# Optimization experiments

Hardware: AMD Instinct MI355X
Metric: run time of the kernel (lower is better)

The kernel has to match this reference:

```python
import jax, jax.numpy as jnp
import numpy as np

B, S, D, H, HD, MLP = 2, 4096, 512, 8, 64, 2048
BLK, C = 128, 32  # Fixed1Pattern(block_size=128), Fixed2Pattern(block_size=128, c=32)
EPS = 1e-6


def _xavier(key, shape, fan_in, fan_out):
    lim = np.sqrt(6.0 / (fan_in + fan_out)).astype(np.float32)
    return jax.random.uniform(key, shape, jnp.float32, -lim, lim)


def setup_inputs() -> dict:
    key = jax.random.key(0)
    ks = jax.random.split(key, 9)
    return {
        "inputs": jax.random.normal(ks[0], (B, S, D), jnp.float32),
        "ln1_scale": jnp.ones((D,), jnp.float32),
        "ln1_bias": jnp.zeros((D,), jnp.float32),
        "wq": _xavier(ks[1], (D, H, HD), D, H * HD),
        "wk": _xavier(ks[2], (D, H, HD), D, H * HD),
        "wv": _xavier(ks[3], (D, H, HD), D, H * HD),
        "wo": _xavier(ks[4], (H, HD, D), H * HD, D),
        "ln2_scale": jnp.ones((D,), jnp.float32),
        "ln2_bias": jnp.zeros((D,), jnp.float32),
        "w1": _xavier(ks[5], (D, MLP), D, MLP),
        "b1": jax.random.normal(ks[6], (MLP,), jnp.float32) * 1e-6,
        "w2": _xavier(ks[7], (MLP, D), MLP, D),
        "b2": jax.random.normal(ks[8], (D,), jnp.float32) * 1e-6,
    }


def _layer_norm(x, scale, bias):
    mu = jnp.mean(x, axis=-1, keepdims=True)
    var = jnp.mean(jnp.square(x - mu), axis=-1, keepdims=True)
    return (x - mu) * jax.lax.rsqrt(var + EPS) * scale + bias


def _sparse_mask():
    # Union of causal Fixed1 (same block) and Fixed2 (last C columns of each block) patterns.
    i = jnp.arange(S)[:, None]
    j = jnp.arange(S)[None, :]
    causal = j <= i
    local = (i // BLK) == (j // BLK)            # Fixed1: within-block
    strided = (j % BLK) >= (BLK - C)            # Fixed2: block-summary columns
    return causal & (local | strided)           # [S, S] bool


def reference(inputs, ln1_scale, ln1_bias, wq, wk, wv, wo,
              ln2_scale, ln2_bias, w1, b1, w2, b2):
    x = _layer_norm(inputs, ln1_scale, ln1_bias)
    q = jnp.einsum("bsd,dhk->bshk", x, wq)
    k = jnp.einsum("bsd,dhk->bshk", x, wk)
    v = jnp.einsum("bsd,dhk->bshk", x, wv)
    scale = 1.0 / np.sqrt(HD).astype(np.float32)
    scores = jnp.einsum("bqhk,bshk->bhqs", q * scale, k)  # [B,H,S,S]
    mask = _sparse_mask()[None, None]
    scores = jnp.where(mask, scores, jnp.float32(-1e9))
    attn = jax.nn.softmax(scores, axis=-1)
    ctx = jnp.einsum("bhqs,bshk->bqhk", attn, v)
    attn_out = jnp.einsum("bqhk,hkd->bqd", ctx, wo)
    x = attn_out + inputs  # residual 1 (dropout deterministic)
    y = _layer_norm(x, ln2_scale, ln2_bias)
    y = jax.nn.gelu(y @ w1 + b1) @ w2 + b2  # MlpBlock
    return x + y
```

## Files before the change

kernel.cpp:

```cpp
#include <hip/hip_runtime.h>
#include <hip/hip_bf16.h>

typedef __attribute__((ext_vector_type(8))) __bf16 bf16x8;
typedef __attribute__((ext_vector_type(8))) short s16x8;
typedef __attribute__((ext_vector_type(4))) float f32x4;

#define NB 2
#define NS 4096
#define ND 512
#define NH 8
#define NHD 64
#define NMLP 2048

__device__ __forceinline__ unsigned short f2b(float f) {
  __hip_bfloat16 h = __float2bfloat16(f);
  return __builtin_bit_cast(unsigned short, h);
}

__device__ __forceinline__ float geluf(float x) {
  float u = 0.7978845608028654f * (x + 0.044715f * x * x * x);
  return x / (1.0f + __expf(-2.0f * u));
}

__device__ __forceinline__ void gload16(const void* g, void* l) {
  __builtin_amdgcn_global_load_lds((const __attribute__((address_space(1))) void*)g,
                                   (__attribute__((address_space(3))) void*)l, 16, 0, 0);
}

__global__ __launch_bounds__(256) void prep_weights(const float* __restrict__ wq,
                                                    const float* __restrict__ wk,
                                                    const float* __restrict__ wv,
                                                    const float* __restrict__ wo,
                                                    const float* __restrict__ w1,
                                                    const float* __restrict__ w2,
                                                    unsigned short* __restrict__ qkvT,
                                                    unsigned short* __restrict__ woT,
                                                    unsigned short* __restrict__ w1T,
                                                    unsigned short* __restrict__ w2T) {
  __shared__ unsigned short lt[64][66];
  const int tile = blockIdx.x, t = threadIdx.x;
  const float* src;
  unsigned short* dst;
  int R, C, tr, tc;
  float sc = 1.0f;
  if (tile < 256) {
    int seg = tile >> 6, tt = tile & 63;
    R = 512; C = 512;
    src = seg == 0 ? wq : seg == 1 ? wk : seg == 2 ? wv : wo;
    dst = (seg < 3) ? (qkvT + ((size_t)seg << 18)) : woT;
    if (seg == 0) sc = 0.125f;
    tr = tt >> 3; tc = tt & 7;
  } else if (tile < 512) {
    int tt = tile - 256;
    R = 512; C = 2048; src = w1; dst = w1T;
    tr = tt >> 5; tc = tt & 31;
  } else {
    int tt = tile - 512;
    R = 2048; C = 512; src = w2; dst = w2T;
    tr = tt >> 3; tc = tt & 7;
  }
  const int r0 = tr * 64, c0 = tc * 64;
  const int fx = t & 15, fy = t >> 4;
#pragma unroll
  for (int p = 0; p < 4; ++p) {
    int rr = p * 16 + fy;
    float4 v = *(const float4*)&src[(size_t)(r0 + rr) * C + c0 + fx * 4];
    lt[rr][fx * 4 + 0] = f2b(v.x * sc);
    lt[rr][fx * 4 + 1] = f2b(v.y * sc);
    lt[rr][fx * 4 + 2] = f2b(v.z * sc);
    lt[rr][fx * 4 + 3] = f2b(v.w * sc);
  }
  __syncthreads();
#pragma unroll
  for (int p = 0; p < 4; ++p) {
    int cc = p * 16 + fy;
    ushort4 o;
    o.x = lt[fx * 4 + 0][cc];
    o.y = lt[fx * 4 + 1][cc];
    o.z = lt[fx * 4 + 2][cc];
    o.w = lt[fx * 4 + 3][cc];
    *(ushort4*)&dst[(size_t)(c0 + cc) * R + r0 + fx * 4] = o;
  }
}

__global__ __launch_bounds__(256) void ln_bf16(const float* __restrict__ x,
                                               const float* __restrict__ g,
                                               const float* __restrict__ bta,
                                               unsigned short* __restrict__ out) {
  const int t = threadIdx.x, l = t & 63, w = t >> 6;
  const size_t row = (size_t)blockIdx.x * 4 + w;
  const float4* xr = (const float4*)(x + row * ND);
  float4 a = xr[l];
  float4 bq = xr[64 + l];
  float s = a.x + a.y + a.z + a.w + bq.x + bq.y + bq.z + bq.w;
  float ss = a.x * a.x + a.y * a.y + a.z * a.z + a.w * a.w +
             bq.x * bq.x + bq.y * bq.y + bq.z * bq.z + bq.w * bq.w;
#pragma unroll
  for (int msk = 1; msk <= 32; msk <<= 1) {
    s += __shfl_xor(s, msk);
    ss += __shfl_xor(ss, msk);
  }
  float mu = s * (1.0f / ND);
  float var = ss * (1.0f / ND) - mu * mu;
  float rr = rsqrtf(var + 1e-6f);
  const float4* g4 = (const float4*)g;
  const float4* b4 = (const float4*)bta;
  float4 g0 = g4[l], g1 = g4[64 + l], b0 = b4[l], b1 = b4[64 + l];
  ushort4 o0, o1;
  o0.x = f2b((a.x - mu) * rr * g0.x + b0.x);
  o0.y = f2b((a.y - mu) * rr * g0.y + b0.y);
  o0.z = f2b((a.z - mu) * rr * g0.z + b0.z);
  o0.w = f2b((a.w - mu) * rr * g0.w + b0.w);
  o1.x = f2b((bq.x - mu) * rr * g1.x + b1.x);
  o1.y = f2b((bq.y - mu) * rr * g1.y + b1.y);
  o1.z = f2b((bq.z - mu) * rr * g1.z + b1.z);
  o1.w = f2b((bq.w - mu) * rr * g1.w + b1.w);
  ushort4* orow = (ushort4*)(out + row * ND);
  orow[l] = o0;
  orow[64 + l] = o1;
}

template <int EPI>
__global__ __launch_bounds__(512, 2) void gemm256(const unsigned short* __restrict__ A,
                                                  const unsigned short* __restrict__ Bt,
                                                  int M, int N, int K,
                                                  unsigned short* __restrict__ ob,
                                                  const float* __restrict__ bias) {
  __shared__ unsigned short lA[2][256 * 64];
  __shared__ unsigned short lB[2][256 * 64];
  const int t = threadIdx.x, l = t & 63, w = t >> 6;
  const int wr = w >> 2, wc = w & 3;
  const int gx = gridDim.x;
  const int nwg = gx * gridDim.y;
  const int fid = blockIdx.y * gx + blockIdx.x;
  const int q8 = nwg >> 3, r8 = nwg & 7, xcd = fid & 7, idx = fid >> 3;
  const int lid = (xcd < r8 ? xcd * (q8 + 1) : r8 * (q8 + 1) + (xcd - r8) * q8) + idx;
  const int bm = lid / gx, bn = lid % gx;
  const size_t rowBytes = (size_t)K * 2;
  const char* Ab = (const char*)A + (size_t)bm * 256 * rowBytes;
  const char* Bb = (const char*)Bt + (size_t)bn * 256 * rowBytes;
  const int srow0 = t >> 3;
  const int scb = (((t & 7) ^ ((t >> 3) & 7)) << 4);
  f32x4 acc[8][4] = {};

  auto stage = [&](int buf, int k0) {
    char* dA = (char*)&lA[buf][0] + t * 16;
    char* dB = (char*)&lB[buf][0] + t * 16;
#pragma unroll
    for (int i = 0; i < 4; ++i) {
      const size_t go = (size_t)(srow0 + i * 64) * rowBytes + 2 * k0 + scb;
      gload16(Ab + go, dA + i * 8192);
      gload16(Bb + go, dB + i * 8192);
    }
  };

  const int nkt = K >> 6;
  stage(0, 0);
  int cur = 0;
  for (int kt = 0; kt < nkt; ++kt) {
    if (kt + 1 < nkt) {
      stage(cur ^ 1, (kt + 1) * 64);
      asm volatile("s_waitcnt vmcnt(8)" ::: "memory");
    } else {
      asm volatile("s_waitcnt vmcnt(0)" ::: "memory");
    }
    __builtin_amdgcn_s_barrier();
    __builtin_amdgcn_sched_barrier(0);
#pragma unroll
    for (int ks = 0; ks < 2; ++ks) {
      const int xg = ((ks * 4 + (l >> 4)) ^ (l & 7)) * 8;
      bf16x8 aF[8], bF[4];
#pragma unroll
      for (int m = 0; m < 8; ++m)
        aF[m] = *(const bf16x8*)&lA[cur][(wr * 128 + m * 16 + (l & 15)) * 64 + xg];
#pragma unroll
      for (int n = 0; n < 4; ++n)
        bF[n] = *(const bf16x8*)&lB[cur][(wc * 64 + n * 16 + (l & 15)) * 64 + xg];
      __builtin_amdgcn_s_setprio(1);
#pragma unroll
      for (int m = 0; m < 8; ++m)
#pragma unroll
        for (int n = 0; n < 4; ++n)
          acc[m][n] = __builtin_amdgcn_mfma_f32_16x16x32_bf16(aF[m], bF[n], acc[m][n], 0, 0, 0);
      __builtin_amdgcn_s_setprio(0);
    }
    asm volatile("s_waitcnt lgkmcnt(0)" ::: "memory");
    __builtin_amdgcn_s_barrier();
    cur ^= 1;
  }
#pragma unroll
  for (int m = 0; m < 8; ++m)
#pragma unroll
    for (int n = 0; n < 4; ++n) {
      int row0 = bm * 256 + wr * 128 + m * 16 + (l >> 4) * 4;
      int col = bn * 256 + wc * 64 + n * 16 + (l & 15);
      if constexpr (EPI == 0) {
        int part = col >> 9, nn = col & 511;
        int hh = nn >> 6, hd = nn & 63;
        int b = row0 >> 12, sidx0 = row0 & 4095;
        if (part < 2) {
#pragma unroll
          for (int j = 0; j < 4; ++j)
            ob[((((size_t)part * NB + b) * NH + hh) * NS + sidx0 + j) * NHD + hd] =
                f2b(acc[m][n][j]);
        } else {
          ushort4 o;
          o.x = f2b(acc[m][n][0]);
          o.y = f2b(acc[m][n][1]);
          o.z = f2b(acc[m][n][2]);
          o.w = f2b(acc[m][n][3]);
          *(ushort4*)&ob[(size_t)2 * NB * NH * NS * NHD +
                         (((size_t)b * NH + hh) * NHD + hd) * NS + sidx0] = o;
        }
      } else {
#pragma unroll
        for (int j = 0; j < 4; ++j) {
          size_t i = (size_t)(row0 + j) * NMLP + col;
          ob[i] = f2b(geluf(acc[m][n][j] + bias[col]));
        }
      }
    }
}

template <int EPI>
__global__ __launch_bounds__(256) void gemm_bt(const unsigned short* __restrict__ A,
                                               const unsigned short* __restrict__ Bt,
                                               int M, int N, int K,
                                               float* __restrict__ of,
                                               const float* __restrict__ addf,
                                               const float* __restrict__ bias) {
  __shared__ unsigned short lA[2][128 * 64];
  __shared__ unsigned short lB[2][128 * 64];
  const int t = threadIdx.x;
  const int l = t & 63, w = t >> 6;
  const int wr = w >> 1, wc = w & 1;
  const int gx = gridDim.x;
  const int nwg = gx * gridDim.y;
  const int fid = blockIdx.y * gx + blockIdx.x;
  const int q8 = nwg >> 3, r8 = nwg & 7, xcd = fid & 7, idx = fid >> 3;
  const int lid = (xcd < r8 ? xcd * (q8 + 1) : r8 * (q8 + 1) + (xcd - r8) * q8) + idx;
  const int bm = lid / gx, bn = lid % gx;
  const size_t rowBytes = (size_t)K * 2;
  const char* Ab = (const char*)A + (size_t)bm * 128 * rowBytes;
  const char* Bb = (const char*)Bt + (size_t)bn * 128 * rowBytes;
  const int srow0 = t >> 3;
  const int scb = (((t & 7) ^ ((t >> 3) & 7)) << 4);
  f32x4 acc[4][4] = {};

  auto stage = [&](int buf, int k0) {
    char* dA = (char*)&lA[buf][0] + t * 16;
    char* dB = (char*)&lB[buf][0] + t * 16;
#pragma unroll
    for (int i = 0; i < 4; ++i) {
      const size_t go = (size_t)(srow0 + i * 32) * rowBytes + 2 * k0 + scb;
      gload16(Ab + go, dA + i * 4096);
      gload16(Bb + go, dB + i * 4096);
    }
  };

  const int nkt = K >> 6;
  stage(0, 0);
  int cur = 0;
  for (int kt = 0; kt < nkt; ++kt) {
    if (kt + 1 < nkt) {
      stage(cur ^ 1, (kt + 1) * 64);
      asm volatile("s_waitcnt vmcnt(8)" ::: "memory");
    } else {
      asm volatile("s_waitcnt vmcnt(0)" ::: "memory");
    }
    __builtin_amdgcn_s_barrier();
    __builtin_amdgcn_sched_barrier(0);
#pragma unroll
    for (int ks = 0; ks < 2; ++ks) {
      const int xg = ((ks * 4 + (l >> 4)) ^ (l & 7)) * 8;
      bf16x8 aF[4], bF[4];
#pragma unroll
      for (int m = 0; m < 4; ++m)
        aF[m] = *(const bf16x8*)&lA[cur][(wr * 64 + m * 16 + (l & 15)) * 64 + xg];
#pragma unroll
      for (int n = 0; n < 4; ++n)
        bF[n] = *(const bf16x8*)&lB[cur][(wc * 64 + n * 16 + (l & 15)) * 64 + xg];
      __builtin_amdgcn_s_setprio(1);
#pragma unroll
      for (int m = 0; m < 4; ++m)
#pragma unroll
        for (int n = 0; n < 4; ++n)
          acc[m][n] = __builtin_amdgcn_mfma_f32_16x16x32_bf16(aF[m], bF[n], acc[m][n], 0, 0, 0);
      __builtin_amdgcn_s_setprio(0);
    }
    asm volatile("s_waitcnt lgkmcnt(0)" ::: "memory");
    __builtin_amdgcn_s_barrier();
    cur ^= 1;
  }
#pragma unroll
  for (int m = 0; m < 4; ++m)
#pragma unroll
    for (int n = 0; n < 4; ++n) {
      int row0 = bm * 128 + wr * 64 + m * 16 + (l >> 4) * 4;
      int col = bn * 128 + wc * 64 + n * 16 + (l & 15);
#pragma unroll
      for (int j = 0; j < 4; ++j) {
        int row = row0 + j;
        float v = acc[m][n][j];
        if constexpr (EPI == 1) {
          size_t i = (size_t)row * ND + col;
          of[i] = v + addf[i];
        } else {
          size_t i = (size_t)row * ND + col;
          of[i] = v + bias[col] + addf[i];
        }
      }
    }
}

__global__ __launch_bounds__(512, 4) void attn_sparse(const unsigned short* __restrict__ qm,
                                                      const unsigned short* __restrict__ km,
                                                      const unsigned short* __restrict__ vTg,
                                                      unsigned short* __restrict__ ctx) {
  __shared__ unsigned short kl[128 * 72];
  __shared__ unsigned short vt[64 * 136];
  __shared__ unsigned short pl[8][16 * 72];
  const int t = threadIdx.x, l = t & 63, w = t >> 6;
  const int bid = blockIdx.x;
  const int hh = bid & 7;
  const int jj = bid >> 3;
  const int b = jj >> 5;
  const int qb = (jj < 32) ? jj : 63 - jj;
  const size_t bh = ((size_t)b * NH + hh) * NS;
  const size_t bhd = ((size_t)b * NH + hh) * NHD;
  const int qrow0 = qb * 128 + w * 16;
  bf16x8 qa[2];
#pragma unroll
  for (int ks = 0; ks < 2; ++ks)
    qa[ks] = *(const bf16x8*)&qm[(bh + qrow0 + (l & 15)) * NHD + ks * 32 + (l >> 4) * 8];
  f32x4 c[4] = {};
  float mrun[4], lrun[4];
#pragma unroll
  for (int j = 0; j < 4; ++j) { mrun[j] = -1e30f; lrun[j] = 0.0f; }

  const int nsum128 = qb >> 2, rem = qb & 3;
  const int nSumCh = nsum128 + (rem ? 1 : 0);
  const int nch = nSumCh + 1;
  const int kkey = t >> 2, kd = (t & 3) * 16;
  const int vd = t >> 3, vk = (t & 7) * 16;

  s16x8 kr0, kr1, vr0, vr1;
  auto issueLoads = [&](int c2) {
    int grK, sV;
    if (c2 < nSumCh) {
      grK = ((c2 << 2) + (kkey >> 5)) * 128 + 96 + (kkey & 31);
      sV = ((c2 << 2) + (vk >> 5)) * 128 + 96 + (vk & 31);
    } else {
      grK = qb * 128 + kkey;
      sV = qb * 128 + vk;
    }
    const unsigned short* kp = &km[(bh + grK) * NHD + kd];
    kr0 = *(const s16x8*)kp;
    kr1 = *(const s16x8*)(kp + 8);
    const unsigned short* vp = &vTg[(bhd + vd) * NS + sV];
    vr0 = *(const s16x8*)vp;
    vr1 = *(const s16x8*)(vp + 8);
  };

  issueLoads(0);
  for (int ch = 0; ch < nch; ++ch) {
    if (ch) {
      asm volatile("s_waitcnt lgkmcnt(0)" ::: "memory");
      __builtin_amdgcn_s_barrier();
    }
    *(s16x8*)&kl[kkey * 72 + kd] = kr0;
    *(s16x8*)&kl[kkey * 72 + kd + 8] = kr1;
    *(s16x8*)&vt[vd * 136 + vk] = vr0;
    *(s16x8*)&vt[vd * 136 + vk + 8] = vr1;
    asm volatile("s_waitcnt lgkmcnt(0)" ::: "memory");
    __builtin_amdgcn_s_barrier();
    __builtin_amdgcn_sched_barrier(0);
    if (ch + 1 < nch) issueLoads(ch + 1);

    const bool isLocal = (ch == nch - 1);
    const bool isRem = (rem != 0) && !isLocal && (ch == nsum128);
    const int nT = isLocal ? (w + 1) : (isRem ? 2 * rem : 8);
    const int nTpl = isLocal ? ((w | 1) + 1) : nT;
    const int nKs = nTpl >> 1;

    f32x4 sf[8];
#pragma unroll
    for (int n = 0; n < 8; ++n) {
      if (n < nT) {
        const bf16x8 k0 = *(const bf16x8*)&kl[(n * 16 + (l & 15)) * 72 + (l >> 4) * 8];
        const bf16x8 k1 = *(const bf16x8*)&kl[(n * 16 + (l & 15)) * 72 + 32 + (l >> 4) * 8];
        f32x4 a = {};
        a = __builtin_amdgcn_mfma_f32_16x16x32_bf16(qa[0], k0, a, 0, 0, 0);
        a = __builtin_amdgcn_mfma_f32_16x16x32_bf16(qa[1], k1, a, 0, 0, 0);
        if (isLocal && n == w) {
#pragma unroll
          for (int j = 0; j < 4; ++j)
            if ((l & 15) > (l >> 4) * 4 + j) a[j] = -1e9f;
        }
        sf[n] = a;
      }
    }
    float cm[4];
#pragma unroll
    for (int j = 0; j < 4; ++j) cm[j] = -1e30f;
#pragma unroll
    for (int n = 0; n < 8; ++n)
      if (n < nT)
#pragma unroll
        for (int j = 0; j < 4; ++j) cm[j] = fmaxf(cm[j], sf[n][j]);
#pragma unroll
    for (int j = 0; j < 4; ++j) {
      cm[j] = fmaxf(cm[j], __shfl_xor(cm[j], 1));
      cm[j] = fmaxf(cm[j], __shfl_xor(cm[j], 2));
      cm[j] = fmaxf(cm[j], __shfl_xor(cm[j], 4));
      cm[j] = fmaxf(cm[j], __shfl_xor(cm[j], 8));
    }
    bool need = false;
#pragma unroll
    for (int j = 0; j < 4; ++j) need |= (cm[j] > mrun[j] + 8.0f);
    if (__any(need)) {
      float al[4];
#pragma unroll
      for (int j = 0; j < 4; ++j) {
        float nm = fmaxf(mrun[j], cm[j]);
        al[j] = __expf(mrun[j] - nm);
        mrun[j] = nm;
      }
#pragma unroll
      for (int n = 0; n < 4; ++n)
#pragma unroll
        for (int j = 0; j < 4; ++j) c[n][j] *= al[j];
#pragma unroll
      for (int j = 0; j < 4; ++j) lrun[j] *= al[j];
    }
    float rs[4] = {0.f, 0.f, 0.f, 0.f};
#pragma unroll
    for (int n = 0; n < 8; ++n)
      if (n < nT)
#pragma unroll
        for (int j = 0; j < 4; ++j) {
          float p = __expf(sf[n][j] - mrun[j]);
          sf[n][j] = p;
          rs[j] += p;
        }
#pragma unroll
    for (int j = 0; j < 4; ++j) {
      rs[j] += __shfl_xor(rs[j], 1);
      rs[j] += __shfl_xor(rs[j], 2);
      rs[j] += __shfl_xor(rs[j], 4);
      rs[j] += __shfl_xor(rs[j], 8);
      lrun[j] += rs[j];
    }
#pragma unroll
    for (int h = 0; h < 2; ++h) {
      if (h * 4 < nTpl) {
#pragma unroll
        for (int n2 = 0; n2 < 4; ++n2) {
          const int n = h * 4 + n2;
#pragma unroll
          for (int j = 0; j < 4; ++j) {
            if (n < nTpl) {
              unsigned short pv = 0;
              if (n < nT) pv = f2b(sf[n][j]);
              pl[w][((l >> 4) * 4 + j) * 72 + n2 * 16 + (l & 15)] = pv;
            }
          }
        }
#pragma unroll
        for (int ks2 = 0; ks2 < 2; ++ks2) {
          const int ks = h * 2 + ks2;
          if (ks < nKs) {
            const bf16x8 pa = *(const bf16x8*)&pl[w][(l & 15) * 72 + ks2 * 32 + (l >> 4) * 8];
#pragma unroll
            for (int nd = 0; nd < 4; ++nd) {
              const bf16x8 vb =
                  *(const bf16x8*)&vt[(nd * 16 + (l & 15)) * 136 + ks * 32 + (l >> 4) * 8];
              c[nd] = __builtin_amdgcn_mfma_f32_16x16x32_bf16(pa, vb, c[nd], 0, 0, 0);
            }
          }
        }
      }
    }
  }
  float rinv[4];
#pragma unroll
  for (int j = 0; j < 4; ++j) rinv[j] = 1.0f / lrun[j];
#pragma unroll
  for (int n = 0; n < 4; ++n)
#pragma unroll
    for (int j = 0; j < 4; ++j) {
      int srow = qrow0 + (l >> 4) * 4 + j;
      int col = n * 16 + (l & 15);
      ctx[((size_t)b * NS + srow) * ND + hh * NHD + col] = f2b(c[n][j] * rinv[j]);
    }
}

extern "C" void kernel_launch(void* const* d_in, const int* in_sizes, int n_in,
                              void* d_out, int out_size, void* d_ws, size_t ws_size,
                              hipStream_t stream) {
  (void)in_sizes; (void)n_in; (void)out_size; (void)ws_size;
  const float* inputs = (const float*)d_in[0];
  const float* ln1s = (const float*)d_in[1];
  const float* ln1b = (const float*)d_in[2];
  const float* wq = (const float*)d_in[3];
  const float* wk = (const float*)d_in[4];
  const float* wv = (const float*)d_in[5];
  const float* wo = (const float*)d_in[6];
  const float* ln2s = (const float*)d_in[7];
  const float* ln2b = (const float*)d_in[8];
  const float* w1 = (const float*)d_in[9];
  const float* b1 = (const float*)d_in[10];
  const float* w2 = (const float*)d_in[11];
  const float* b2 = (const float*)d_in[12];
  float* out = (float*)d_out;

  unsigned short* xln = (unsigned short*)d_ws;
  unsigned short* xln2 = xln + (size_t)8192 * 512;
  unsigned short* ctx = xln2 + (size_t)8192 * 512;
  unsigned short* qkv = ctx + (size_t)8192 * 512;
  float* xres = (float*)(qkv + (size_t)3 * 8192 * 512);
  unsigned short* hbuf = (unsigned short*)(xres + (size_t)8192 * 512);
  unsigned short* qkvT = hbuf + (size_t)8192 * 2048;
  unsigned short* woT = qkvT + (size_t)1536 * 512;
  unsigned short* w1T = woT + (size_t)512 * 512;
  unsigned short* w2T = w1T + (size_t)2048 * 512;

  prep_weights<<<768, 256, 0, stream>>>(wq, wk, wv, wo, w1, w2, qkvT, woT, w1T, w2T);
  ln_bf16<<<2048, 256, 0, stream>>>(inputs, ln1s, ln1b, xln);
  gemm256<0><<<dim3(6, 32), 512, 0, stream>>>(xln, qkvT, 8192, 1536, 512, qkv, nullptr);
  attn_sparse<<<512, 512, 0, stream>>>(qkv, qkv + (size_t)8192 * 512,
                                       qkv + (size_t)2 * 8192 * 512, ctx);
  gemm_bt<1><<<dim3(4, 64), 256, 0, stream>>>(ctx, woT, 8192, 512, 512,
                                              xres, inputs, nullptr);
  ln_bf16<<<2048, 256, 0, stream>>>(xres, ln2s, ln2b, xln2);
  gemm256<2><<<dim3(8, 32), 512, 0, stream>>>(xln2, w1T, 8192, 2048, 512, hbuf, b1);
  gemm_bt<3><<<dim3(4, 64), 256, 0, stream>>>(hbuf, w2T, 8192, 512, 2048,
                                              out, xres, b2);
}
```

Before: 163.0 us.

## Split attention blocks into half-query workgroups, read V from global, widen gemm_bt to 8 waves

The attention kernel now runs 1024 workgroups of 4 waves, each covering half of a 128-row query block, so there is more parallelism and finer load balancing. K is staged in an XOR-swizzled LDS tile with no padding. V is no longer staged in LDS and the PV MFMA operands are read straight from global memory. The gemm_bt kernel moves to 8 waves per 128x128 tile, with each wave holding a 64x32 accumulator and fewer staging loads per thread. The trade-off is higher global/L2 traffic for V and possible latency stalls in the PV loop, in exchange for higher occupancy and less LDS use.

```diff
diff --git a/kernel.cpp b/kernel.cpp
--- a/kernel.cpp
+++ b/kernel.cpp
@@ -223,7 +223,7 @@
 }
 
 template <int EPI>
-__global__ __launch_bounds__(256) void gemm_bt(const unsigned short* __restrict__ A,
+__global__ __launch_bounds__(512) void gemm_bt(const unsigned short* __restrict__ A,
                                                const unsigned short* __restrict__ Bt,
                                                int M, int N, int K,
                                                float* __restrict__ of,
@@ -233,7 +233,7 @@
   __shared__ unsigned short lB[2][128 * 64];
   const int t = threadIdx.x;
   const int l = t & 63, w = t >> 6;
-  const int wr = w >> 1, wc = w & 1;
+  const int wr = w >> 2, wc = w & 3;
   const int gx = gridDim.x;
   const int nwg = gx * gridDim.y;
   const int fid = blockIdx.y * gx + blockIdx.x;
@@ -243,18 +243,18 @@
   const size_t rowBytes = (size_t)K * 2;
   const char* Ab = (const char*)A + (size_t)bm * 128 * rowBytes;
   const char* Bb = (const char*)Bt + (size_t)bn * 128 * rowBytes;
-  const int srow0 = t >> 3;
+  const int sr0 = t >> 3;
   const int scb = (((t & 7) ^ ((t >> 3) & 7)) << 4);
-  f32x4 acc[4][4] = {};
+  f32x4 acc[4][2] = {};
 
   auto stage = [&](int buf, int k0) {
     char* dA = (char*)&lA[buf][0] + t * 16;
     char* dB = (char*)&lB[buf][0] + t * 16;
 #pragma unroll
-    for (int i = 0; i < 4; ++i) {
-      const size_t go = (size_t)(srow0 + i * 32) * rowBytes + 2 * k0 + scb;
-      gload16(Ab + go, dA + i * 4096);
-      gload16(Bb + go, dB + i * 4096);
+    for (int i = 0; i < 2; ++i) {
+      const size_t go = (size_t)(sr0 + i * 64) * rowBytes + 2 * k0 + scb;
+      gload16(Ab + go, dA + i * 8192);
+      gload16(Bb + go, dB + i * 8192);
     }
   };
 
@@ -264,7 +264,7 @@
   for (int kt = 0; kt < nkt; ++kt) {
     if (kt + 1 < nkt) {
       stage(cur ^ 1, (kt + 1) * 64);
-      asm volatile("s_waitcnt vmcnt(8)" ::: "memory");
+      asm volatile("s_waitcnt vmcnt(4)" ::: "memory");
     } else {
       asm volatile("s_waitcnt vmcnt(0)" ::: "memory");
     }
@@ -273,18 +273,18 @@
 #pragma unroll
     for (int ks = 0; ks < 2; ++ks) {
       const int xg = ((ks * 4 + (l >> 4)) ^ (l & 7)) * 8;
-      bf16x8 aF[4], bF[4];
+      bf16x8 aF[4], bF[2];
 #pragma unroll
       for (int m = 0; m < 4; ++m)
         aF[m] = *(const bf16x8*)&lA[cur][(wr * 64 + m * 16 + (l & 15)) * 64 + xg];
 #pragma unroll
-      for (int n = 0; n < 4; ++n)
-        bF[n] = *(const bf16x8*)&lB[cur][(wc * 64 + n * 16 + (l & 15)) * 64 + xg];
+      for (int n = 0; n < 2; ++n)
+        bF[n] = *(const bf16x8*)&lB[cur][(wc * 32 + n * 16 + (l & 15)) * 64 + xg];
       __builtin_amdgcn_s_setprio(1);
 #pragma unroll
       for (int m = 0; m < 4; ++m)
 #pragma unroll
-        for (int n = 0; n < 4; ++n)
+        for (int n = 0; n < 2; ++n)
           acc[m][n] = __builtin_amdgcn_mfma_f32_16x16x32_bf16(aF[m], bF[n], acc[m][n], 0, 0, 0);
       __builtin_amdgcn_s_setprio(0);
     }
@@ -295,9 +295,9 @@
 #pragma unroll
   for (int m = 0; m < 4; ++m)
 #pragma unroll
-    for (int n = 0; n < 4; ++n) {
+    for (int n = 0; n < 2; ++n) {
       int row0 = bm * 128 + wr * 64 + m * 16 + (l >> 4) * 4;
-      int col = bn * 128 + wc * 64 + n * 16 + (l & 15);
+      int col = bn * 128 + wc * 32 + n * 16 + (l & 15);
 #pragma unroll
       for (int j = 0; j < 4; ++j) {
         int row = row0 + j;
@@ -313,22 +313,25 @@
     }
 }
 
-__global__ __launch_bounds__(512, 4) void attn_sparse(const unsigned short* __restrict__ qm,
+__global__ __launch_bounds__(256, 6) void attn_sparse(const unsigned short* __restrict__ qm,
                                                       const unsigned short* __restrict__ km,
                                                       const unsigned short* __restrict__ vTg,
                                                       unsigned short* __restrict__ ctx) {
-  __shared__ unsigned short kl[128 * 72];
-  __shared__ unsigned short vt[64 * 136];
-  __shared__ unsigned short pl[8][16 * 72];
+  __shared__ unsigned short kl[128 * 64];
+  __shared__ unsigned short pl[4][16 * 64];
   const int t = threadIdx.x, l = t & 63, w = t >> 6;
   const int bid = blockIdx.x;
   const int hh = bid & 7;
   const int jj = bid >> 3;
-  const int b = jj >> 5;
-  const int qb = (jj < 32) ? jj : 63 - jj;
+  const int b = jj >> 6;
+  const int rr = jj & 63;
+  const int half = rr & 1;
+  const int qb0 = rr >> 1;
+  const int qb = half ? (31 - qb0) : qb0;
+  const int wp = half * 4 + w;
   const size_t bh = ((size_t)b * NH + hh) * NS;
   const size_t bhd = ((size_t)b * NH + hh) * NHD;
-  const int qrow0 = qb * 128 + w * 16;
+  const int qrow0 = qb * 128 + half * 64 + w * 16;
   bf16x8 qa[2];
 #pragma unroll
   for (int ks = 0; ks < 2; ++ks)
@@ -341,25 +344,17 @@
   const int nsum128 = qb >> 2, rem = qb & 3;
   const int nSumCh = nsum128 + (rem ? 1 : 0);
   const int nch = nSumCh + 1;
-  const int kkey = t >> 2, kd = (t & 3) * 16;
-  const int vd = t >> 3, vk = (t & 7) * 16;
-
-  s16x8 kr0, kr1, vr0, vr1;
+  const int sr0 = t >> 3, sg = t & 7;
+
+  s16x8 kr[4];
   auto issueLoads = [&](int c2) {
-    int grK, sV;
-    if (c2 < nSumCh) {
-      grK = ((c2 << 2) + (kkey >> 5)) * 128 + 96 + (kkey & 31);
-      sV = ((c2 << 2) + (vk >> 5)) * 128 + 96 + (vk & 31);
-    } else {
-      grK = qb * 128 + kkey;
-      sV = qb * 128 + vk;
-    }
-    const unsigned short* kp = &km[(bh + grK) * NHD + kd];
-    kr0 = *(const s16x8*)kp;
-    kr1 = *(const s16x8*)(kp + 8);
-    const unsigned short* vp = &vTg[(bhd + vd) * NS + sV];
-    vr0 = *(const s16x8*)vp;
-    vr1 = *(const s16x8*)(vp + 8);
+#pragma unroll
+    for (int i = 0; i < 4; ++i) {
+      const int r = sr0 + 32 * i;
+      const int grK = (c2 < nSumCh) ? ((c2 * 4 + (r >> 5)) * 128 + 96 + (r & 31))
+                                    : (qb * 128 + r);
+      kr[i] = *(const s16x8*)&km[(bh + grK) * NHD + sg * 8];
+    }
   };
 
   issueLoads(0);
@@ -368,10 +363,11 @@
       asm volatile("s_waitcnt lgkmcnt(0)" ::: "memory");
       __builtin_amdgcn_s_barrier();
     }
-    *(s16x8*)&kl[kkey * 72 + kd] = kr0;
-    *(s16x8*)&kl[kkey * 72 + kd + 8] = kr1;
-    *(s16x8*)&vt[vd * 136 + vk] = vr0;
-    *(s16x8*)&vt[vd * 136 + vk + 8] = vr1;
+#pragma unroll
+    for (int i = 0; i < 4; ++i) {
+      const int r = sr0 + 32 * i;
+      *(s16x8*)&kl[r * 64 + ((sg ^ (r & 7)) << 3)] = kr[i];
+    }
     asm volatile("s_waitcnt lgkmcnt(0)" ::: "memory");
     __builtin_amdgcn_s_barrier();
     __builtin_amdgcn_sched_barrier(0);
@@ -379,20 +375,21 @@
 
     const bool isLocal = (ch == nch - 1);
     const bool isRem = (rem != 0) && !isLocal && (ch == nsum128);
-    const int nT = isLocal ? (w + 1) : (isRem ? 2 * rem : 8);
-    const int nTpl = isLocal ? ((w | 1) + 1) : nT;
+    const int nT = isLocal ? (wp + 1) : (isRem ? 2 * rem : 8);
+    const int nTpl = isLocal ? ((wp | 1) + 1) : nT;
     const int nKs = nTpl >> 1;
 
     f32x4 sf[8];
 #pragma unroll
     for (int n = 0; n < 8; ++n) {
       if (n < nT) {
-        const bf16x8 k0 = *(const bf16x8*)&kl[(n * 16 + (l & 15)) * 72 + (l >> 4) * 8];
-        const bf16x8 k1 = *(const bf16x8*)&kl[(n * 16 + (l & 15)) * 72 + 32 + (l >> 4) * 8];
+        const int row = n * 16 + (l & 15);
+        const bf16x8 k0 = *(const bf16x8*)&kl[row * 64 + ((((l >> 4)) ^ (l & 7)) << 3)];
+        const bf16x8 k1 = *(const bf16x8*)&kl[row * 64 + (((4 + (l >> 4)) ^ (l & 7)) << 3)];
         f32x4 a = {};
         a = __builtin_amdgcn_mfma_f32_16x16x32_bf16(qa[0], k0, a, 0, 0, 0);
         a = __builtin_amdgcn_mfma_f32_16x16x32_bf16(qa[1], k1, a, 0, 0, 0);
-        if (isLocal && n == w) {
+        if (isLocal && n == wp) {
 #pragma unroll
           for (int j = 0; j < 4; ++j)
             if ((l & 15) > (l >> 4) * 4 + j) a[j] = -1e9f;
@@ -452,29 +449,33 @@
       lrun[j] += rs[j];
     }
 #pragma unroll
-    for (int h = 0; h < 2; ++h) {
-      if (h * 4 < nTpl) {
+    for (int h2 = 0; h2 < 2; ++h2) {
+      if (h2 * 4 < nTpl) {
 #pragma unroll
         for (int n2 = 0; n2 < 4; ++n2) {
-          const int n = h * 4 + n2;
+          const int n = h2 * 4 + n2;
 #pragma unroll
           for (int j = 0; j < 4; ++j) {
             if (n < nTpl) {
               unsigned short pv = 0;
               if (n < nT) pv = f2b(sf[n][j]);
-              pl[w][((l >> 4) * 4 + j) * 72 + n2 * 16 + (l & 15)] = pv;
+              const int rowp = (l >> 4) * 4 + j;
+              const int grp = (n2 * 2 + ((l & 15) >> 3)) ^ (rowp & 7);
+              pl[w][rowp * 64 + grp * 8 + (l & 7)] = pv;
             }
           }
         }
 #pragma unroll
         for (int ks2 = 0; ks2 < 2; ++ks2) {
-          const int ks = h * 2 + ks2;
+          const int ks = h2 * 2 + ks2;
           if (ks < nKs) {
-            const bf16x8 pa = *(const bf16x8*)&pl[w][(l & 15) * 72 + ks2 * 32 + (l >> 4) * 8];
+            const bf16x8 pa =
+                *(const bf16x8*)&pl[w][(l & 15) * 64 + (((ks2 * 4 + (l >> 4)) ^ (l & 7)) << 3)];
+            const int segBase = (ch < nSumCh) ? ((ch * 4 + ks) * 128 + 96) : (qb * 128 + ks * 32);
 #pragma unroll
             for (int nd = 0; nd < 4; ++nd) {
-              const bf16x8 vb =
-                  *(const bf16x8*)&vt[(nd * 16 + (l & 15)) * 136 + ks * 32 + (l >> 4) * 8];
+              const bf16x8 vb = *(const bf16x8*)&vTg[(bhd + nd * 16 + (l & 15)) * NS +
+                                                     segBase + (l >> 4) * 8];
               c[nd] = __builtin_amdgcn_mfma_f32_16x16x32_bf16(pa, vb, c[nd], 0, 0, 0);
             }
           }
@@ -528,12 +529,12 @@
   prep_weights<<<768, 256, 0, stream>>>(wq, wk, wv, wo, w1, w2, qkvT, woT, w1T, w2T);
   ln_bf16<<<2048, 256, 0, stream>>>(inputs, ln1s, ln1b, xln);
   gemm256<0><<<dim3(6, 32), 512, 0, stream>>>(xln, qkvT, 8192, 1536, 512, qkv, nullptr);
-  attn_sparse<<<512, 512, 0, stream>>>(qkv, qkv + (size_t)8192 * 512,
-                                       qkv + (size_t)2 * 8192 * 512, ctx);
-  gemm_bt<1><<<dim3(4, 64), 256, 0, stream>>>(ctx, woT, 8192, 512, 512,
+  attn_sparse<<<1024, 256, 0, stream>>>(qkv, qkv + (size_t)8192 * 512,
+                                        qkv + (size_t)2 * 8192 * 512, ctx);
+  gemm_bt<1><<<dim3(4, 64), 512, 0, stream>>>(ctx, woT, 8192, 512, 512,
                                               xres, inputs, nullptr);
   ln_bf16<<<2048, 256, 0, stream>>>(xres, ln2s, ln2b, xln2);
   gemm256<2><<<dim3(8, 32), 512, 0, stream>>>(xln2, w1T, 8192, 2048, 512, hbuf, b1);
-  gemm_bt<3><<<dim3(4, 64), 256, 0, stream>>>(hbuf, w2T, 8192, 512, 2048,
+  gemm_bt<3><<<dim3(4, 64), 512, 0, stream>>>(hbuf, w2T, 8192, 512, 2048,
                                               out, xres, b2);
 }
```

Measured after the change: 344.0 us. 111% more time.
